# Performance work log

Measured on AMD Instinct MI355X. Metric: run time of the kernel, lower is better.

## Reference

```python
import jax, jax.numpy as jnp
import numpy as np

EMB = 1024
N_HEADS = 16
HEAD = EMB // N_HEADS
EPS = 1e-5


def layernorm(x, g, b):
    mu = jnp.mean(x, axis=-1, keepdims=True)
    var = jnp.var(x, axis=-1, keepdims=True)
    return (x - mu) * jax.lax.rsqrt(var + EPS) * g + b


def setup_inputs() -> dict:
    key = jax.random.key(0)
    ks = jax.random.split(key, 12)
    s = lambda fan_in: 1.0 / np.sqrt(fan_in)
    return {
        "x": jax.random.normal(ks[0], (8, 1024, EMB), dtype=jnp.float32),
        "ln1_g": jnp.ones((EMB,), jnp.float32),
        "ln1_b": jnp.zeros((EMB,), jnp.float32),
        "wq": jax.random.uniform(ks[1], (EMB, EMB), jnp.float32, -s(EMB), s(EMB)),
        "wk": jax.random.uniform(ks[2], (EMB, EMB), jnp.float32, -s(EMB), s(EMB)),
        "wv": jax.random.uniform(ks[3], (EMB, EMB), jnp.float32, -s(EMB), s(EMB)),
        "w_proj": jax.random.uniform(ks[4], (EMB, EMB), jnp.float32, -s(EMB), s(EMB)),
        "b_proj": jnp.zeros((EMB,), jnp.float32),
        "ln2_g": jnp.ones((EMB,), jnp.float32),
        "ln2_b": jnp.zeros((EMB,), jnp.float32),
        "w1": jax.random.uniform(ks[5], (EMB, 4 * EMB), jnp.float32, -s(EMB), s(EMB)),
        "b1": jnp.zeros((4 * EMB,), jnp.float32),
        "w2": jax.random.uniform(ks[6], (4 * EMB, EMB), jnp.float32, -s(4 * EMB), s(4 * EMB)),
        "b2": jnp.zeros((EMB,), jnp.float32),
    }


def reference(x, ln1_g, ln1_b, wq, wk, wv, w_proj, b_proj, ln2_g, ln2_b, w1, b1, w2, b2):
    B, T, E = x.shape
    h = layernorm(x, ln1_g, ln1_b)
    # per-head no-bias projections == one big matmul then split into heads
    q = (h @ wq).reshape(B, T, N_HEADS, HEAD).transpose(0, 2, 1, 3)  # [B,H,T,D]
    k = (h @ wk).reshape(B, T, N_HEADS, HEAD).transpose(0, 2, 1, 3)
    v = (h @ wv).reshape(B, T, N_HEADS, HEAD).transpose(0, 2, 1, 3)
    scores = jnp.einsum("bhqd,bhkd->bhqk", q, k) * (HEAD ** -0.5)
    causal = jnp.tril(jnp.ones((T, T), dtype=bool))
    scores = jnp.where(causal, scores, -jnp.inf)
    wei = jax.nn.softmax(scores, axis=-1)  # dropout is identity at eval
    attn = jnp.einsum("bhqk,bhkd->bhqd", wei, v)
    attn = attn.transpose(0, 2, 1, 3).reshape(B, T, E)
    out = x + attn @ w_proj + b_proj
    h2 = layernorm(out, ln2_g, ln2_b)
    mlp = jax.nn.gelu(h2 @ w1 + b1, approximate=False) @ w2 + b2
    return out + mlp
```

## Files before the change

### kernel.cpp

```cpp
#include <hip/hip_runtime.h>
#include <hip/hip_bf16.h>

#define EMB 1024
#define NH 16
#define HD 64
#define BATCH 8
#define SEQ 1024
#define ROWS (BATCH*SEQ)

typedef unsigned short ushort_t;
typedef __attribute__((ext_vector_type(8))) short bf16x8;
typedef __attribute__((ext_vector_type(4))) float f32x4;
typedef __attribute__((ext_vector_type(16))) float f32x16;

__device__ __forceinline__ float bf2f(ushort_t u){
    union { unsigned int i; float f; } v; v.i = ((unsigned int)u) << 16; return v.f;
}
__device__ __forceinline__ ushort_t f2bf(float f){
    unsigned int u = __float_as_uint(f);
    unsigned int r = (u + 0x7FFFu + ((u >> 16) & 1u)) >> 16;
    return (ushort_t)r;
}
__device__ __forceinline__ void gload16(const ushort_t* g, ushort_t* l){
    __builtin_amdgcn_global_load_lds(
        (const __attribute__((address_space(1))) void*)g,
        (__attribute__((address_space(3))) void*)l,
        16, 0, 0);
}
__device__ __forceinline__ void tile_sync(){
    asm volatile("s_waitcnt vmcnt(0)" ::: "memory");
    __builtin_amdgcn_s_barrier();
    asm volatile("" ::: "memory");
}
__device__ __forceinline__ float gelu_f(float v){
    float x = fabsf(v) * 0.70710678118654752f;
    float t = __builtin_amdgcn_rcpf(1.0f + 0.3275911f * x);
    float poly = t*(0.254829592f + t*(-0.284496736f + t*(1.421413741f + t*(-1.453152027f + t*1.061405429f))));
    float erfa = 1.0f - poly * __expf(-x*x);
    float erfv = (v >= 0.f) ? erfa : -erfa;
    return 0.5f * v * (1.0f + erfv);
}

__global__ __launch_bounds__(256) void prep_kernel(const float* __restrict__ x,
                                                   const float* __restrict__ ln1_g,
                                                   const float* __restrict__ ln1_b,
                                                   ushort_t* __restrict__ h1,
                                                   const float* __restrict__ wq,
                                                   const float* __restrict__ wk,
                                                   const float* __restrict__ wv,
                                                   const float* __restrict__ w_proj,
                                                   const float* __restrict__ w1,
                                                   const float* __restrict__ w2,
                                                   ushort_t* __restrict__ wqkv_t,
                                                   ushort_t* __restrict__ wproj_t,
                                                   ushort_t* __restrict__ w1_t,
                                                   ushort_t* __restrict__ w2_t){
    int bid = blockIdx.x;
    int tid = threadIdx.x;
    if (bid < ROWS){
        __shared__ float ss[4], qq[4];
        __shared__ float mu_s, sc_s;
        const float* xr = x + (size_t)bid * EMB;
        float4 f = *(const float4*)(xr + tid*4);
        float v[4] = {f.x, f.y, f.z, f.w};
        float s = v[0]+v[1]+v[2]+v[3];
        float q = v[0]*v[0]+v[1]*v[1]+v[2]*v[2]+v[3]*v[3];
        #pragma unroll
        for (int o = 32; o > 0; o >>= 1){ s += __shfl_down(s, o); q += __shfl_down(q, o); }
        int wave = tid >> 6, lane = tid & 63;
        if (lane == 0){ ss[wave] = s; qq[wave] = q; }
        __syncthreads();
        if (tid == 0){
            float S = ss[0]+ss[1]+ss[2]+ss[3];
            float Q = qq[0]+qq[1]+qq[2]+qq[3];
            float mu = S * (1.0f/EMB);
            float var = Q * (1.0f/EMB) - mu*mu;
            mu_s = mu; sc_s = rsqrtf(var + 1e-5f);
        }
        __syncthreads();
        float mu = mu_s, sc = sc_s;
        float4 gu = *(const float4*)(ln1_g + tid*4);
        float4 bu = *(const float4*)(ln1_b + tid*4);
        ushort4 o4;
        o4.x = f2bf((v[0]-mu)*sc*gu.x + bu.x);
        o4.y = f2bf((v[1]-mu)*sc*gu.y + bu.y);
        o4.z = f2bf((v[2]-mu)*sc*gu.z + bu.z);
        o4.w = f2bf((v[3]-mu)*sc*gu.w + bu.w);
        *(ushort4*)(h1 + (size_t)bid*EMB + tid*4) = o4;
    } else {
        __shared__ ushort_t t[32][33];
        int j = bid - ROWS;
        const float* in; ushort_t* out; int K, N, bx, by;
        if (j < 3072){
            int which = j >> 10, jj = j & 1023;
            in = (which == 0) ? wq : (which == 1) ? wk : wv;
            out = wqkv_t + (size_t)which * 1024 * 1024;
            K = 1024; N = 1024; bx = jj & 31; by = jj >> 5;
        } else if (j < 4096){
            int jj = j - 3072;
            in = w_proj; out = wproj_t; K = 1024; N = 1024; bx = jj & 31; by = jj >> 5;
        } else if (j < 8192){
            int jj = j - 4096;
            in = w1; out = w1_t; K = 1024; N = 4096; bx = jj & 127; by = jj >> 7;
        } else {
            int jj = j - 8192;
            in = w2; out = w2_t; K = 4096; N = 1024; bx = jj & 31; by = jj >> 5;
        }
        int tx = tid & 31, ty = tid >> 5;
        #pragma unroll
        for (int r = 0; r < 4; ++r)
            t[ty + r*8][tx] = f2bf(in[(size_t)(by*32 + ty + r*8) * N + bx*32 + tx]);
        __syncthreads();
        #pragma unroll
        for (int r = 0; r < 4; ++r)
            out[(size_t)(bx*32 + ty + r*8) * K + by*32 + tx] = t[tx][ty + r*8];
    }
}

__global__ __launch_bounds__(256) void ln_kernel(const float* __restrict__ xin,
                                                 const float* __restrict__ g,
                                                 const float* __restrict__ bia,
                                                 ushort_t* __restrict__ out){
    int row = blockIdx.x;
    int tid = threadIdx.x;
    const float* x = xin + (size_t)row * EMB;
    float4 f = *(const float4*)(x + tid*4);
    float v[4] = {f.x, f.y, f.z, f.w};
    float s = v[0]+v[1]+v[2]+v[3];
    float q = v[0]*v[0]+v[1]*v[1]+v[2]*v[2]+v[3]*v[3];
    #pragma unroll
    for (int o = 32; o > 0; o >>= 1){ s += __shfl_down(s, o); q += __shfl_down(q, o); }
    __shared__ float ss[4], qq[4];
    __shared__ float mu_s, sc_s;
    int wave = tid >> 6, lane = tid & 63;
    if (lane == 0){ ss[wave] = s; qq[wave] = q; }
    __syncthreads();
    if (tid == 0){
        float S = ss[0]+ss[1]+ss[2]+ss[3];
        float Q = qq[0]+qq[1]+qq[2]+qq[3];
        float mu = S * (1.0f/EMB);
        float var = Q * (1.0f/EMB) - mu*mu;
        mu_s = mu; sc_s = rsqrtf(var + 1e-5f);
    }
    __syncthreads();
    float mu = mu_s, sc = sc_s;
    float4 gu = *(const float4*)(g + tid*4);
    float4 bu = *(const float4*)(bia + tid*4);
    ushort4 o4;
    o4.x = f2bf((v[0]-mu)*sc*gu.x + bu.x);
    o4.y = f2bf((v[1]-mu)*sc*gu.y + bu.y);
    o4.z = f2bf((v[2]-mu)*sc*gu.z + bu.z);
    o4.w = f2bf((v[3]-mu)*sc*gu.w + bu.w);
    *(ushort4*)(out + (size_t)row*EMB + tid*4) = o4;
}

template<int MODE>
__global__ __launch_bounds__(512, 2) void gemm_kernel(const ushort_t* __restrict__ A,
                                                      const ushort_t* __restrict__ Bt,
                                                      const float* __restrict__ bias,
                                                      const float* __restrict__ resid,
                                                      void* __restrict__ out,
                                                      int M, int N, int K){
    __shared__ ushort_t As[2][256*64];
    __shared__ ushort_t Bs[2][128*64];
    int tid = threadIdx.x;
    int lane = tid & 63, wave = tid >> 6;
    int l31 = lane & 31, half = lane >> 5;
    int wm = wave >> 2, wn = wave & 3;
    int bid = blockIdx.x;
    int m0 = (bid & 31) * 256, n0 = (bid >> 5) * 128;

    f32x16 acc[4];
    #pragma unroll
    for (int i=0;i<4;i++)
        #pragma unroll
        for (int r=0;r<16;r++) acc[i][r] = 0.f;

    int lr  = lane >> 3;
    int lch = lane & 7;
    const ushort_t* gA = A  + (size_t)(m0 + wave*32 + lr)*K + (lch ^ lr)*8;
    const ushort_t* gB = Bt + (size_t)(n0 + wave*16 + lr)*K + (lch ^ lr)*8;
    int sx = lane & 7;
    int NT = K >> 6;

    auto stage = [&](int b, int k0){
        ushort_t* lA = &As[b][(wave*32)*64];
        ushort_t* lB = &Bs[b][(wave*16)*64];
        #pragma unroll
        for (int i = 0; i < 4; ++i) gload16(gA + (size_t)(i*8)*K + k0, lA + i*8*64);
        #pragma unroll
        for (int p = 0; p < 2; ++p) gload16(gB + (size_t)(p*8)*K + k0, lB + p*8*64);
    };

    stage(0, 0);
    tile_sync();
    int cur = 0;
    for (int t = 0; t < NT; ++t){
        if (t + 1 < NT) stage(cur ^ 1, (t + 1) << 6);
        const ushort_t* Ac = As[cur];
        const ushort_t* Bc = Bs[cur];
        #pragma unroll
        for (int s = 0; s < 4; ++s){
            int ch = ((s<<1) | half) ^ sx;
            bf16x8 af[4];
            #pragma unroll
            for (int i=0;i<4;i++) af[i] = *(const bf16x8*)&Ac[(wm*128 + i*32 + l31)*64 + ch*8];
            bf16x8 bfr = *(const bf16x8*)&Bc[(wn*32 + l31)*64 + ch*8];
            #pragma unroll
            for (int i=0;i<4;i++)
                acc[i] = __builtin_amdgcn_mfma_f32_32x32x16_bf16(af[i], bfr, acc[i], 0,0,0);
        }
        if (t + 1 < NT) tile_sync();
        cur ^= 1;
    }

    int n = n0 + wn*32 + l31;
    float bn = (MODE != 0) ? bias[n] : 0.f;
    int rowoff = 4*half;
    #pragma unroll
    for (int i=0;i<4;i++){
        #pragma unroll
        for (int reg=0; reg<16; ++reg){
            int m = m0 + wm*128 + i*32 + (reg&3) + 8*(reg>>2) + rowoff;
            float v = acc[i][reg];
            size_t idx = (size_t)m*N + n;
            if (MODE == 0){
                ((ushort_t*)out)[idx] = f2bf(v);
            } else if (MODE == 1 || MODE == 3){
                v += bn + resid[idx];
                ((float*)out)[idx] = v;
            } else {
                ((ushort_t*)out)[idx] = f2bf(gelu_f(v + bn));
            }
        }
    }
}

__global__ __launch_bounds__(256) void attn_kernel(const ushort_t* __restrict__ qkv,
                                                   ushort_t* __restrict__ attn_out){
    __shared__ ushort_t Qs[128*64];
    __shared__ ushort_t Ks[64*64];
    __shared__ ushort_t Vts[64][72];
    __shared__ ushort_t Ps[128*64];

    int tid = threadIdx.x;
    int lane = tid & 63, wave = tid >> 6;
    int quad = lane >> 4, l15 = lane & 15;
    int pair = blockIdx.x;
    int bh = blockIdx.y;
    int b = bh >> 4, h = bh & 15;
    size_t tb = (size_t)b * SEQ;

    int lr = lane >> 3, lch = lane & 7;
    int tr = tid >> 3;
    int tc = (tid & 7) * 8;
    int sw_w = tid & 7;
    int sx = l15 & 7;

    for (int t = 0; t < 2; ++t){
        int qi = t ? (7 - pair) : pair;

        {
            const ushort_t* gq = qkv + (size_t)(tb + qi*128 + wave*32 + lr)*3072 + h*64 + (lch^lr)*8;
            ushort_t* lq = &Qs[(wave*32)*64];
            #pragma unroll
            for (int p = 0; p < 4; ++p)
                gload16(gq + (size_t)(p*8)*3072, lq + p*8*64);
        }

        f32x4 o_acc[4][2];
        #pragma unroll
        for (int i=0;i<4;i++)
            #pragma unroll
            for (int j=0;j<2;j++) o_acc[i][j] = (f32x4){0.f,0.f,0.f,0.f};
        float m_st[2] = {-1e30f, -1e30f};
        float l_st[2] = {0.f, 0.f};

        int nj = 2*qi + 2;
        for (int j = 0; j < nj; ++j){
            {
                const ushort_t* gk = qkv + (size_t)(tb + j*64 + wave*16 + lr)*3072 + 1024 + h*64 + (lch^lr)*8;
                ushort_t* lk = &Ks[(wave*16)*64];
                gload16(gk, lk);
                gload16(gk + (size_t)8*3072, lk + 8*64);
            }
            #pragma unroll
            for (int p = 0; p < 2; ++p){
                int r = tr + p*32;
                bf16x8 vv = *(const bf16x8*)(qkv + (size_t)(tb + j*64 + r)*3072 + 2048 + h*64 + tc);
                int kcol = r ^ (sw_w << 3);
                #pragma unroll
                for (int c = 0; c < 8; ++c) Vts[tc + c][kcol] = (ushort_t)vv[c];
            }
            __syncthreads();

            f32x4 st[4][2];
            #pragma unroll
            for (int mt=0;mt<4;mt++)
                #pragma unroll
                for (int nt=0;nt<2;nt++) st[mt][nt] = (f32x4){0.f,0.f,0.f,0.f};
            #pragma unroll
            for (int kf = 0; kf < 2; ++kf){
                int ch = (kf*4 + quad) ^ sx;
                bf16x8 ak[4], bq[2];
                #pragma unroll
                for (int mt=0;mt<4;mt++) ak[mt] = *(const bf16x8*)&Ks[(mt*16 + l15)*64 + ch*8];
                #pragma unroll
                for (int nt=0;nt<2;nt++) bq[nt] = *(const bf16x8*)&Qs[(wave*32 + nt*16 + l15)*64 + ch*8];
                #pragma unroll
                for (int mt=0;mt<4;mt++)
                    #pragma unroll
                    for (int nt=0;nt<2;nt++)
                        st[mt][nt] = __builtin_amdgcn_mfma_f32_16x16x32_bf16(ak[mt], bq[nt], st[mt][nt], 0,0,0);
            }

            bool need_mask = (j >= 2*qi);
            #pragma unroll
            for (int mt=0;mt<4;mt++)
                #pragma unroll
                for (int nt=0;nt<2;nt++)
                    #pragma unroll
                    for (int r=0;r<4;r++){
                        float s = st[mt][nt][r] * 0.125f;
                        if (need_mask){
                            int kg = j*64 + mt*16 + quad*4 + r;
                            int qg = qi*128 + wave*32 + nt*16 + l15;
                            if (kg > qg) s = -1e30f;
                        }
                        st[mt][nt][r] = s;
                    }

            #pragma unroll
            for (int nt = 0; nt < 2; ++nt){
                float mx = st[0][nt][0];
                #pragma unroll
                for (int mt=0;mt<4;mt++)
                    #pragma unroll
                    for (int r=0;r<4;r++) mx = fmaxf(mx, st[mt][nt][r]);
                mx = fmaxf(mx, __shfl_xor(mx, 16));
                mx = fmaxf(mx, __shfl_xor(mx, 32));
                float mnew = fmaxf(m_st[nt], mx);
                float al = __expf(m_st[nt] - mnew);
                float ps = 0.f;
                #pragma unroll
                for (int mt=0;mt<4;mt++)
                    #pragma unroll
                    for (int r=0;r<4;r++){
                        float p = __expf(st[mt][nt][r] - mnew);
                        st[mt][nt][r] = p;
                        ps += p;
                    }
                ps += __shfl_xor(ps, 16);
                ps += __shfl_xor(ps, 32);
                l_st[nt] = l_st[nt]*al + ps;
                m_st[nt] = mnew;
                #pragma unroll
                for (int mtd=0;mtd<4;mtd++)
                    #pragma unroll
                    for (int r=0;r<4;r++) o_acc[mtd][nt][r] *= al;
                #pragma unroll
                for (int mt=0;mt<4;mt++){
                    int slot = (mt*2 + (quad>>1)) ^ sx;
                    ushort4 pk;
                    pk.x = f2bf(st[mt][nt][0]); pk.y = f2bf(st[mt][nt][1]);
                    pk.z = f2bf(st[mt][nt][2]); pk.w = f2bf(st[mt][nt][3]);
                    *(ushort4*)&Ps[(wave*32 + nt*16 + l15)*64 + slot*8 + (quad&1)*4] = pk;
                }
            }

            #pragma unroll
            for (int kf = 0; kf < 2; ++kf){
                bf16x8 av[4], bp[2];
                #pragma unroll
                for (int mtd=0;mtd<4;mtd++){
                    int d = mtd*16 + l15;
                    int col = (kf*32 + quad*8) ^ (((d >> 3) & 7) << 3);
                    av[mtd] = *(const bf16x8*)&Vts[d][col];
                }
                #pragma unroll
                for (int nt=0;nt<2;nt++){
                    int ch = (kf*4 + quad) ^ sx;
                    bp[nt] = *(const bf16x8*)&Ps[(wave*32 + nt*16 + l15)*64 + ch*8];
                }
                #pragma unroll
                for (int mtd=0;mtd<4;mtd++)
                    #pragma unroll
                    for (int nt=0;nt<2;nt++)
                        o_acc[mtd][nt] = __builtin_amdgcn_mfma_f32_16x16x32_bf16(av[mtd], bp[nt], o_acc[mtd][nt], 0,0,0);
            }
            __syncthreads();
        }

        #pragma unroll
        for (int nt = 0; nt < 2; ++nt){
            float inv = 1.0f / l_st[nt];
            size_t tok = tb + qi*128 + wave*32 + nt*16 + l15;
            #pragma unroll
            for (int mtd = 0; mtd < 4; ++mtd){
                ushort4 ok;
                ok.x = f2bf(o_acc[mtd][nt][0]*inv); ok.y = f2bf(o_acc[mtd][nt][1]*inv);
                ok.z = f2bf(o_acc[mtd][nt][2]*inv); ok.w = f2bf(o_acc[mtd][nt][3]*inv);
                *(ushort4*)(attn_out + tok*EMB + h*64 + mtd*16 + quad*4) = ok;
            }
        }
    }
}

extern "C" void kernel_launch(void* const* d_in, const int* in_sizes, int n_in,
                              void* d_out, int out_size, void* d_ws, size_t ws_size,
                              hipStream_t stream){
    const float* x      = (const float*)d_in[0];
    const float* ln1_g  = (const float*)d_in[1];
    const float* ln1_b  = (const float*)d_in[2];
    const float* wq     = (const float*)d_in[3];
    const float* wk     = (const float*)d_in[4];
    const float* wv     = (const float*)d_in[5];
    const float* w_proj = (const float*)d_in[6];
    const float* b_proj = (const float*)d_in[7];
    const float* ln2_g  = (const float*)d_in[8];
    const float* ln2_b  = (const float*)d_in[9];
    const float* w1     = (const float*)d_in[10];
    const float* b1     = (const float*)d_in[11];
    const float* w2     = (const float*)d_in[12];
    const float* b2     = (const float*)d_in[13];
    float* outp = (float*)d_out;

    char* ws = (char*)d_ws;
    size_t off = 0;
    auto alloc = [&](size_t bytes)->char*{ char* p = ws + off; off += (bytes + 255) & ~255ULL; return p; };
    ushort_t* wqkv_t = (ushort_t*)alloc((size_t)3072*1024*2);
    ushort_t* wproj_t= (ushort_t*)alloc((size_t)1024*1024*2);
    ushort_t* w1_t   = (ushort_t*)alloc((size_t)4096*1024*2);
    ushort_t* w2_t   = (ushort_t*)alloc((size_t)1024*4096*2);
    ushort_t* qkv    = (ushort_t*)alloc((size_t)ROWS*3072*2);
    ushort_t* hbuf   = (ushort_t*)alloc((size_t)ROWS*1024*2);
    float*    out32  = (float*)  alloc((size_t)ROWS*1024*4);
    ushort_t* mid    = (ushort_t*)alloc((size_t)ROWS*4096*2);
    ushort_t* h1 = hbuf;
    ushort_t* attn = hbuf;
    ushort_t* h2 = qkv;

    dim3 blk(256);
    dim3 gblk(512);
    prep_kernel<<<dim3(20480), blk, 0, stream>>>(x, ln1_g, ln1_b, h1,
                                                 wq, wk, wv, w_proj, w1, w2,
                                                 wqkv_t, wproj_t, w1_t, w2_t);
    gemm_kernel<0><<<dim3(32*(3072/128)), gblk, 0, stream>>>(h1, wqkv_t, nullptr, nullptr, qkv, ROWS, 3072, 1024);
    attn_kernel<<<dim3(4,128), blk, 0, stream>>>(qkv, attn);
    gemm_kernel<1><<<dim3(32*(1024/128)), gblk, 0, stream>>>(attn, wproj_t, b_proj, x, out32, ROWS, 1024, 1024);
    ln_kernel<<<ROWS, blk, 0, stream>>>(out32, ln2_g, ln2_b, h2);
    gemm_kernel<2><<<dim3(32*(4096/128)), gblk, 0, stream>>>(h2, w1_t, b1, nullptr, mid, ROWS, 4096, 1024);
    gemm_kernel<3><<<dim3(32*(1024/128)), gblk, 0, stream>>>(mid, w2_t, b2, out32, outp, ROWS, 1024, 4096);
}
```

Before: 509.9 us.

## Rewrite GEMM with 16x16x32 MFMA, fragment-major LDS layout and wider MLP tile

```diff
diff --git a/kernel.cpp b/kernel.cpp
--- a/kernel.cpp
+++ b/kernel.cpp
@@ -11,7 +11,6 @@
 typedef unsigned short ushort_t;
 typedef __attribute__((ext_vector_type(8))) short bf16x8;
 typedef __attribute__((ext_vector_type(4))) float f32x4;
-typedef __attribute__((ext_vector_type(16))) float f32x16;
 
 __device__ __forceinline__ float bf2f(ushort_t u){
     union { unsigned int i; float f; } v; v.i = ((unsigned int)u) << 16; return v.f;
@@ -27,7 +26,12 @@
         (__attribute__((address_space(3))) void*)l,
         16, 0, 0);
 }
-__device__ __forceinline__ void tile_sync(){
+__device__ __forceinline__ void fence_barrier(){
+    asm volatile("" ::: "memory");
+    __builtin_amdgcn_s_barrier();
+    asm volatile("" ::: "memory");
+}
+__device__ __forceinline__ void drain_barrier(){
     asm volatile("s_waitcnt vmcnt(0)" ::: "memory");
     __builtin_amdgcn_s_barrier();
     asm volatile("" ::: "memory");
@@ -154,83 +158,103 @@
     *(ushort4*)(out + (size_t)row*EMB + tid*4) = o4;
 }
 
-template<int MODE>
-__global__ __launch_bounds__(512, 2) void gemm_kernel(const ushort_t* __restrict__ A,
-                                                      const ushort_t* __restrict__ Bt,
-                                                      const float* __restrict__ bias,
-                                                      const float* __restrict__ resid,
-                                                      void* __restrict__ out,
-                                                      int M, int N, int K){
-    __shared__ ushort_t As[2][256*64];
-    __shared__ ushort_t Bs[2][128*64];
+template<int MODE, int NBL>
+__global__ __launch_bounds__(512, 2) void gemm8_kernel(const ushort_t* __restrict__ A,
+                                                       const ushort_t* __restrict__ Bt,
+                                                       const float* __restrict__ bias,
+                                                       const float* __restrict__ resid,
+                                                       void* __restrict__ out,
+                                                       int M, int N, int K){
+    constexpr int BN = NBL * 64;
+    __shared__ ushort_t As[2][16384];
+    __shared__ ushort_t Bs[2][NBL*4096];
+
     int tid = threadIdx.x;
-    int lane = tid & 63, wave = tid >> 6;
-    int l31 = lane & 31, half = lane >> 5;
-    int wm = wave >> 2, wn = wave & 3;
+    int lane = tid & 63, w = tid >> 6;
+    int l15 = lane & 15, lq = lane >> 4;
+    int wm = w >> 2, wn = w & 3;
     int bid = blockIdx.x;
-    int m0 = (bid & 31) * 256, n0 = (bid >> 5) * 128;
-
-    f32x16 acc[4];
+    int m0 = (bid & 31) * 256, n0 = (bid >> 5) * BN;
+
+    f32x4 acc[8][NBL];
     #pragma unroll
-    for (int i=0;i<4;i++)
-        #pragma unroll
-        for (int r=0;r<16;r++) acc[i][r] = 0.f;
-
-    int lr  = lane >> 3;
-    int lch = lane & 7;
-    const ushort_t* gA = A  + (size_t)(m0 + wave*32 + lr)*K + (lch ^ lr)*8;
-    const ushort_t* gB = Bt + (size_t)(n0 + wave*16 + lr)*K + (lch ^ lr)*8;
-    int sx = lane & 7;
+    for (int i=0;i<8;i++)
+        #pragma unroll
+        for (int j=0;j<NBL;j++) acc[i][j] = (f32x4){0.f,0.f,0.f,0.f};
+
+    const ushort_t* pA = A  + (size_t)(m0 + (w>>1)*16 + l15)*K + (w&1)*32 + lq*8;
+    const ushort_t* pB = Bt + (size_t)(n0 + (w>>1)*16 + l15)*K + (w&1)*32 + lq*8;
+
+    auto stage = [&](int buf, int k0){
+        #pragma unroll
+        for (int i = 0; i < 4; ++i)
+            gload16(pA + (size_t)i*64*K + k0, &As[buf][i*4096 + w*512]);
+        #pragma unroll
+        for (int i = 0; i < NBL; ++i)
+            gload16(pB + (size_t)i*64*K + k0, &Bs[buf][i*4096 + w*512]);
+    };
+
+    stage(0, 0);
+    drain_barrier();
+
     int NT = K >> 6;
-
-    auto stage = [&](int b, int k0){
-        ushort_t* lA = &As[b][(wave*32)*64];
-        ushort_t* lB = &Bs[b][(wave*16)*64];
-        #pragma unroll
-        for (int i = 0; i < 4; ++i) gload16(gA + (size_t)(i*8)*K + k0, lA + i*8*64);
-        #pragma unroll
-        for (int p = 0; p < 2; ++p) gload16(gB + (size_t)(p*8)*K + k0, lB + p*8*64);
-    };
-
-    stage(0, 0);
-    tile_sync();
-    int cur = 0;
     for (int t = 0; t < NT; ++t){
+        int cur = t & 1;
+        const ushort_t* Ab = As[cur];
+        const ushort_t* Bb = Bs[cur];
         if (t + 1 < NT) stage(cur ^ 1, (t + 1) << 6);
-        const ushort_t* Ac = As[cur];
-        const ushort_t* Bc = Bs[cur];
-        #pragma unroll
-        for (int s = 0; s < 4; ++s){
-            int ch = ((s<<1) | half) ^ sx;
-            bf16x8 af[4];
-            #pragma unroll
-            for (int i=0;i<4;i++) af[i] = *(const bf16x8*)&Ac[(wm*128 + i*32 + l31)*64 + ch*8];
-            bf16x8 bfr = *(const bf16x8*)&Bc[(wn*32 + l31)*64 + ch*8];
-            #pragma unroll
-            for (int i=0;i<4;i++)
-                acc[i] = __builtin_amdgcn_mfma_f32_32x32x16_bf16(af[i], bfr, acc[i], 0,0,0);
-        }
-        if (t + 1 < NT) tile_sync();
-        cur ^= 1;
+
+        bf16x8 bfr[NBL][2];
+        #pragma unroll
+        for (int nb=0;nb<NBL;nb++)
+            #pragma unroll
+            for (int fk=0;fk<2;fk++)
+                bfr[nb][fk] = *(const bf16x8*)&Bb[(((wn*NBL + nb)*2 + fk)*64 + lane)*8];
+
+        #pragma unroll
+        for (int p = 0; p < 4; ++p){
+            bf16x8 af[2][2];
+            #pragma unroll
+            for (int q=0;q<2;q++)
+                #pragma unroll
+                for (int fk=0;fk<2;fk++)
+                    af[q][fk] = *(const bf16x8*)&Ab[(((wm*8 + 2*p + q)*2 + fk)*64 + lane)*8];
+            __builtin_amdgcn_s_setprio(1);
+            #pragma unroll
+            for (int q=0;q<2;q++)
+                #pragma unroll
+                for (int nb=0;nb<NBL;nb++){
+                    acc[2*p+q][nb] = __builtin_amdgcn_mfma_f32_16x16x32_bf16(af[q][0], bfr[nb][0], acc[2*p+q][nb], 0,0,0);
+                    acc[2*p+q][nb] = __builtin_amdgcn_mfma_f32_16x16x32_bf16(af[q][1], bfr[nb][1], acc[2*p+q][nb], 0,0,0);
+                }
+            __builtin_amdgcn_s_setprio(0);
+            if (p < 3) fence_barrier();
+        }
+        drain_barrier();
     }
 
-    int n = n0 + wn*32 + l31;
-    float bn = (MODE != 0) ? bias[n] : 0.f;
-    int rowoff = 4*half;
+    int n_base = n0 + wn*(NBL*16);
+    int m_base = m0 + wm*128 + lq*4;
+    float bn[NBL];
     #pragma unroll
-    for (int i=0;i<4;i++){
-        #pragma unroll
-        for (int reg=0; reg<16; ++reg){
-            int m = m0 + wm*128 + i*32 + (reg&3) + 8*(reg>>2) + rowoff;
-            float v = acc[i][reg];
-            size_t idx = (size_t)m*N + n;
-            if (MODE == 0){
-                ((ushort_t*)out)[idx] = f2bf(v);
-            } else if (MODE == 1 || MODE == 3){
-                v += bn + resid[idx];
-                ((float*)out)[idx] = v;
-            } else {
-                ((ushort_t*)out)[idx] = f2bf(gelu_f(v + bn));
+    for (int nb=0;nb<NBL;nb++) bn[nb] = (MODE != 0) ? bias[n_base + nb*16 + l15] : 0.f;
+    #pragma unroll
+    for (int mb=0;mb<8;mb++){
+        #pragma unroll
+        for (int nb=0;nb<NBL;nb++){
+            int n = n_base + nb*16 + l15;
+            #pragma unroll
+            for (int r=0;r<4;r++){
+                int m = m_base + mb*16 + r;
+                float v = acc[mb][nb][r];
+                size_t idx = (size_t)m*N + n;
+                if (MODE == 0){
+                    ((ushort_t*)out)[idx] = f2bf(v);
+                } else if (MODE == 1 || MODE == 3){
+                    ((float*)out)[idx] = v + bn[nb] + resid[idx];
+                } else {
+                    ((ushort_t*)out)[idx] = f2bf(gelu_f(v + bn[nb]));
+                }
             }
         }
     }
@@ -445,10 +469,10 @@
     prep_kernel<<<dim3(20480), blk, 0, stream>>>(x, ln1_g, ln1_b, h1,
                                                  wq, wk, wv, w_proj, w1, w2,
                                                  wqkv_t, wproj_t, w1_t, w2_t);
-    gemm_kernel<0><<<dim3(32*(3072/128)), gblk, 0, stream>>>(h1, wqkv_t, nullptr, nullptr, qkv, ROWS, 3072, 1024);
+    gemm8_kernel<0,2><<<dim3(32*(3072/128)), gblk, 0, stream>>>(h1, wqkv_t, nullptr, nullptr, qkv, ROWS, 3072, 1024);
     attn_kernel<<<dim3(4,128), blk, 0, stream>>>(qkv, attn);
-    gemm_kernel<1><<<dim3(32*(1024/128)), gblk, 0, stream>>>(attn, wproj_t, b_proj, x, out32, ROWS, 1024, 1024);
+    gemm8_kernel<1,2><<<dim3(32*(1024/128)), gblk, 0, stream>>>(attn, wproj_t, b_proj, x, out32, ROWS, 1024, 1024);
     ln_kernel<<<ROWS, blk, 0, stream>>>(out32, ln2_g, ln2_b, h2);
-    gemm_kernel<2><<<dim3(32*(4096/128)), gblk, 0, stream>>>(h2, w1_t, b1, nullptr, mid, ROWS, 4096, 1024);
-    gemm_kernel<3><<<dim3(32*(1024/128)), gblk, 0, stream>>>(mid, w2_t, b2, out32, outp, ROWS, 1024, 4096);
-}
+    gemm8_kernel<2,4><<<dim3(32*(4096/256)), gblk, 0, stream>>>(h2, w1_t, b1, nullptr, mid, ROWS, 4096, 1024);
+    gemm8_kernel<3,2><<<dim3(32*(1024/128)), gblk, 0, stream>>>(mid, w2_t, b2, out32, outp, ROWS, 1024, 4096);
+}
```

Result: slower. 630.7 us (+23.7%).
